# Performance work log

Hardware: AMD Instinct MI355X
Metric: run time of the kernel (lower is better)

The kernel has to match this reference:

```python
import jax, jax.numpy as jnp
from jax import lax
import numpy as np

IMG_H = 14; IMG_W = 14
L = 21   # num_labels
M = 5    # num_mixture_filters
KL = 50  # local conv kernel
PL = 25  # local conv padding
HO = IMG_H + 2 * PL - KL + 1  # 15, locally-connected output size
CH = [(64, 3), (64, 64), (128, 64), (128, 128), (256, 128), (256, 256), (256, 256),
      (512, 256), (512, 512), (512, 512), (512, 512), (512, 512), (512, 512)]
DIL = [1, 1, 1, 1, 1, 1, 1, 1, 1, 1, 2, 2, 2]


def setup_inputs() -> dict:
    keys = iter(jax.random.split(jax.random.key(0), 80))
    def rnd(shape, s=0.05):
        return jax.random.normal(next(keys), shape, dtype=jnp.float32) * s
    d = {"x": jax.random.normal(next(keys), (2, 3, IMG_H, IMG_W), dtype=jnp.float32)}
    for i, (o, c) in enumerate(CH):
        d["w%d" % (i + 1)] = rnd((o, c, 3, 3))
        d["b%d" % (i + 1)] = rnd((o,))
    d["wf1"] = rnd((4096, 512, 7, 7), s=0.01); d["bf1"] = rnd((4096,))
    d["wf2"] = rnd((4096, 4096, 1, 1), s=0.01); d["bf2"] = rnd((4096,))
    d["wf3"] = rnd((L, 4096, 1, 1), s=0.01); d["bf3"] = rnd((L,))
    d["wl"] = rnd((HO, HO, L, L, KL, KL), s=0.01)  # per-position local-conv weights
    d["bl"] = rnd((L, HO, HO))
    d["wa"] = rnd((L, L)); d["ba"] = rnd((L,))
    d["wm"] = rnd((L * M, L, 9, 9, L)); d["bm"] = rnd((L * M,))
    d["wb"] = rnd((L * M, L * M)); d["bb"] = rnd((L * M,))
    return d


def _conv2d(x, w, b, pad, dil=1):
    y = lax.conv_general_dilated(x, w, (1, 1), [(pad, pad), (pad, pad)],
                                 rhs_dilation=(dil, dil),
                                 dimension_numbers=("NCHW", "OIHW", "NCHW"))
    return y + b[None, :, None, None]


def _maxpool2(x):
    return lax.reduce_window(x, -jnp.inf, lax.max, (1, 1, 2, 2), (1, 1, 2, 2), "VALID")


def _upsample_bilinear_ac(x, H, W):
    # UpsamplingBilinear2d == bilinear with align_corners=True
    def lerp(t, n_in, n_out, axis):
        src = jnp.arange(n_out, dtype=jnp.float32) * (float(n_in - 1) / max(n_out - 1, 1))
        i0 = jnp.clip(jnp.floor(src).astype(jnp.int32), 0, max(n_in - 2, 0))
        i1 = jnp.minimum(i0 + 1, n_in - 1)
        f = src - i0.astype(jnp.float32)
        shp = [1] * t.ndim; shp[axis] = n_out
        f = f.reshape(shp).astype(t.dtype)
        return jnp.take(t, i0, axis=axis) * (1 - f) + jnp.take(t, i1, axis=axis) * f
    return lerp(lerp(x, x.shape[2], H, 2), x.shape[3], W, 3)


def reference(x, w1, b1, w2, b2, w3, b3, w4, b4, w5, b5, w6, b6, w7, b7, w8, b8,
              w9, b9, w10, b10, w11, b11, w12, b12, w13, b13,
              wf1, bf1, wf2, bf2, wf3, bf3, wl, bl, wa, ba, wm, bm, wb, bb):
    ws = [w1, w2, w3, w4, w5, w6, w7, w8, w9, w10, w11, w12, w13]
    bs = [b1, b2, b3, b4, b5, b6, b7, b8, b9, b10, b11, b12, b13]
    h = x
    for i in range(13):
        h = jax.nn.relu(_conv2d(h, ws[i], bs[i], pad=DIL[i], dil=DIL[i]))
        if i in (1, 3, 6):  # MaxPool2d after VGG blocks 1,2,3
            h = _maxpool2(h)
    h = jax.nn.relu(_conv2d(h, wf1, bf1, pad=12, dil=4))  # 7x7 dilated FC-conv
    h = jax.nn.relu(_conv2d(h, wf2, bf2, pad=0))
    h = _conv2d(h, wf3, bf3, pad=0)                       # -> [B, L, h', w']
    h = jax.nn.sigmoid(_upsample_bilinear_ac(h, IMG_H, IMG_W))
    # Conv2dLocal: locally-connected 50x50 conv, per-position weights
    xp = jnp.pad(h, ((0, 0), (0, 0), (PL, PL), (PL, PL)))
    idx = jnp.arange(HO)[:, None] + jnp.arange(KL)[None, :]  # [HO, KL]
    p = xp[:, :, idx, :][:, :, :, :, idx]  # [B, C, HO, KL, HO, KL]
    h = jnp.einsum("bcisjt,ijocst->boij", p, wl) + bl[None]  # [B, L, HO, HO]
    # Linear over the label (channel) axis
    h = jnp.einsum("bchw,oc->bohw", h, wa) + ba[None, :, None, None]
    # Conv3d mixture head: label axis unsqueezed to depth-1 last spatial dim,
    # kernel (9, 9, L) with padding (4, 4, L//2) -> depth out = 1
    y = lax.conv_general_dilated(h[..., None], wm, (1, 1, 1),
                                 [(4, 4), (4, 4), (L // 2, L // 2)],
                                 dimension_numbers=("NCDHW", "OIDHW", "NCDHW"))
    h = y[..., 0] + bm[None, :, None, None]  # [B, L*M, HO, HO]
    h = jnp.einsum("bchw,oc->bohw", h, wb) + bb[None, :, None, None]
    # BlockMinPooling(kernel=M) over last dim: split into (M, W//M), min over block axis
    B_, C_, H_, W_ = h.shape
    h = h.reshape(B_, C_, H_, M, W_ // M).min(axis=3)  # [B, L*M, HO, HO//M]
    # AvgPool2d(kernel=1, stride=1, divisor_override=1) is the identity
    return jax.nn.softmax(h, axis=1)
```

## Files before the change

kernel.cpp:

```cpp
#include <hip/hip_runtime.h>
#include <math.h>

#define HO 15
#define LBL 21
#define MIX 5
#define LM 105
#define NB 256
#define NT 512
#define GSZ (NB * NT)
#define NWV (GSZ / 64)

struct Params {
    const float* x;
    const float* w[14]; const float* b[14];
    const float *wf1, *bf1, *wf2, *bf2, *wf3, *bf3;
    const float *wl, *bl, *wa, *ba, *wm, *bm, *wb, *bb;
    float *A, *B, *v, *h1, *h3, *out;
    int* bar;
};

__device__ __forceinline__ float max4(float a, float b, float c, float d) {
    return fmaxf(fmaxf(a, b), fmaxf(c, d));
}

__device__ __forceinline__ void gbar(int* bar, int id) {
    __syncthreads();
    if (threadIdx.x == 0) {
        __threadfence();
        int* c = bar + id * 16;
        __hip_atomic_fetch_add(c, 1, __ATOMIC_RELAXED, __HIP_MEMORY_SCOPE_AGENT);
        while (__hip_atomic_load(c, __ATOMIC_RELAXED, __HIP_MEMORY_SCOPE_AGENT) < NB)
            __builtin_amdgcn_s_sleep(16);
        (void)__hip_atomic_load(c, __ATOMIC_ACQUIRE, __HIP_MEMORY_SCOPE_AGENT);
    }
    __syncthreads();
}

template <int Cin, int Cout, int Hi, int H, int POOL>
__device__ void wconv(const float* __restrict__ in, const float* __restrict__ w,
                      const float* __restrict__ bias, float* __restrict__ out,
                      int gw, int lane) {
    constexpr int CPL = Cin / 64;
    for (int idx = gw; idx < 2 * Cout * H * H; idx += NWV) {
        int x = idx % H; int t = idx / H;
        int y = t % H; t /= H;
        int o = t % Cout; int b = t / Cout;
        const float* ip = in + (size_t)b * Cin * Hi * Hi;
        float acc = 0.f;
#pragma unroll
        for (int cc = 0; cc < CPL; ++cc) {
            int c = lane + 64 * cc;
            const float* ic = ip + (size_t)c * Hi * Hi;
            const float* wc = w + ((size_t)o * Cin + c) * 9;
#pragma unroll
            for (int ky = 0; ky < 3; ++ky) {
                int yy = y + ky - 1;
                if (yy < 0 || yy >= H) continue;
#pragma unroll
                for (int kx = 0; kx < 3; ++kx) {
                    int xx = x + kx - 1;
                    if (xx < 0 || xx >= H) continue;
                    float val;
                    if (POOL == 1) {
                        val = ic[yy * Hi + xx];
                    } else {
                        const float* q = ic + (2 * yy) * Hi + 2 * xx;
                        val = max4(q[0], q[1], q[Hi], q[Hi + 1]);
                    }
                    acc += val * wc[ky * 3 + kx];
                }
            }
        }
#pragma unroll
        for (int off = 32; off; off >>= 1) acc += __shfl_xor(acc, off);
        if (lane == 0) out[idx] = fmaxf(acc + bias[o], 0.f);
    }
}

template <int Cin, int ACT, int POOLIN>
__device__ void mvtap(const float* __restrict__ in, const float* __restrict__ w,
                      const float* __restrict__ bias, float* __restrict__ out,
                      int Cout, int S, int F, float* sin, int tid, int gw, int lane) {
    if (POOLIN) {
        for (int c = tid; c < 2 * Cin; c += NT) {
            const float* q = in + (size_t)c * 9;
            sin[c] = max4(q[0], q[1], q[3], q[4]);
        }
    } else {
        for (int c = tid; c < 2 * Cin; c += NT) sin[c] = in[c];
    }
    __syncthreads();
    constexpr int K = Cin / 64;
    for (int o = gw; o < Cout; o += NWV) {
        const float* wp = w + ((size_t)o * Cin + lane) * S + F;
        float wr[K];
#pragma unroll
        for (int k = 0; k < K; ++k) wr[k] = wp[(size_t)(64 * S) * k];
        float a0 = 0.f, a1 = 0.f;
#pragma unroll
        for (int k = 0; k < K; ++k) {
            a0 += wr[k] * sin[lane + 64 * k];
            a1 += wr[k] * sin[Cin + lane + 64 * k];
        }
#pragma unroll
        for (int off = 32; off; off >>= 1) {
            a0 += __shfl_xor(a0, off);
            a1 += __shfl_xor(a1, off);
        }
        if (lane == 0) {
            float bv = bias[o];
            a0 += bv; a1 += bv;
            if (ACT == 1) { a0 = fmaxf(a0, 0.f); a1 = fmaxf(a1, 0.f); }
            if (ACT == 2) { a0 = 1.f / (1.f + expf(-a0)); a1 = 1.f / (1.f + expf(-a1)); }
            out[o] = a0;
            out[Cout + o] = a1;
        }
    }
}

template <int Cin, int ACT>
__device__ void mvrow4(const float* __restrict__ in, const float* __restrict__ w,
                       const float* __restrict__ bias, float* __restrict__ out,
                       int Cout, float* sin, int tid, int gw, int lane) {
    for (int c = tid; c < 2 * Cin; c += NT) sin[c] = in[c];
    __syncthreads();
    constexpr int K4 = Cin / 256;
    const float4* s0 = (const float4*)sin;
    const float4* s1 = (const float4*)(sin + Cin);
    for (int o = gw; o < Cout; o += NWV) {
        const float4* wp = (const float4*)(w + (size_t)o * Cin) + lane;
        float4 wr[K4];
#pragma unroll
        for (int k = 0; k < K4; ++k) wr[k] = wp[64 * k];
        float a0 = 0.f, a1 = 0.f;
#pragma unroll
        for (int k = 0; k < K4; ++k) {
            float4 xv = s0[lane + 64 * k];
            float4 yv = s1[lane + 64 * k];
            a0 += wr[k].x * xv.x + wr[k].y * xv.y + wr[k].z * xv.z + wr[k].w * xv.w;
            a1 += wr[k].x * yv.x + wr[k].y * yv.y + wr[k].z * yv.z + wr[k].w * yv.w;
        }
#pragma unroll
        for (int off = 32; off; off >>= 1) {
            a0 += __shfl_xor(a0, off);
            a1 += __shfl_xor(a1, off);
        }
        if (lane == 0) {
            float bv = bias[o];
            a0 += bv; a1 += bv;
            if (ACT == 1) { a0 = fmaxf(a0, 0.f); a1 = fmaxf(a1, 0.f); }
            if (ACT == 2) { a0 = 1.f / (1.f + expf(-a0)); a1 = 1.f / (1.f + expf(-a1)); }
            out[o] = a0;
            out[Cout + o] = a1;
        }
    }
}

__device__ void localstage(const float* __restrict__ wl, const float* __restrict__ bl,
                           const float* __restrict__ v, float* __restrict__ h1,
                           int gw, int lane) {
    int e1 = lane + 64, e2 = lane + 128, e3 = lane + 192;
    int off0 = (lane / 14) * 50 + lane % 14;
    int off1 = (e1 / 14) * 50 + e1 % 14;
    int off2 = (e2 / 14) * 50 + e2 % 14;
    int off3 = (lane < 4) ? ((e3 / 14) * 50 + e3 % 14) : off0;
    float m3 = (lane < 4) ? 1.f : 0.f;
    for (int wk = gw; wk < LBL * HO * HO; wk += NWV) {
        int j = wk % HO; int t1 = wk / HO;
        int i = t1 % HO; int o = t1 / HO;
        int s0 = 25 - i, t0 = 25 - j;
        size_t base_ij = ((size_t)(i * HO + j) * LBL + o) * LBL;
        const float* pij = wl + base_ij * 2500 + s0 * 50 + t0;
        float a0 = 0.f, a1 = 0.f;
#pragma unroll 7
        for (int c = 0; c < LBL; ++c) {
            const float* p = pij + (size_t)c * 2500;
            float part = p[off0] + p[off1] + p[off2] + m3 * p[off3];
            a0 += v[c] * part;
            a1 += v[LBL + c] * part;
        }
#pragma unroll
        for (int off = 32; off; off >>= 1) {
            a0 += __shfl_xor(a0, off);
            a1 += __shfl_xor(a1, off);
        }
        if (lane == 0) {
            float bv = bl[(o * HO + i) * HO + j];
            h1[(size_t)(0 * LBL + o) * 225 + i * HO + j] = a0 + bv;
            h1[(size_t)(1 * LBL + o) * 225 + i * HO + j] = a1 + bv;
        }
    }
}

__device__ void ninestage(const float* __restrict__ h1, const float* __restrict__ wa,
                          const float* __restrict__ ba, const float* __restrict__ wm,
                          const float* __restrict__ bm, float* __restrict__ h3,
                          float* smem, int tid) {
    int blk = blockIdx.x;
    if (blk >= 2 * LM) return;
    float* s1 = smem;
    float* s2 = smem + 4725;
    float* sw = smem + 9450;
    float* swa = smem + 11151;
    int b = blk / LM, o = blk % LM;
    for (int k = tid; k < 4725; k += NT) s1[k] = h1[(size_t)b * 4725 + k];
    for (int k = tid; k < 441; k += NT) swa[k] = wa[k];
    for (int k = tid; k < 1701; k += NT) sw[k] = wm[((size_t)o * 1701 + k) * LBL + 10];
    __syncthreads();
    for (int k = tid; k < 4725; k += NT) {
        int c = k / 225, pix = k % 225;
        float acc = ba[c];
#pragma unroll 7
        for (int c2 = 0; c2 < LBL; ++c2)
            acc += swa[c * LBL + c2] * s1[c2 * 225 + pix];
        s2[k] = acc;
    }
    __syncthreads();
    if (tid >= 225) return;
    int i = tid / HO, j = tid % HO;
    float acc = bm[o];
    for (int c = 0; c < LBL; ++c) {
        const float* wp = sw + c * 81;
        const float* hp = s2 + c * 225;
#pragma unroll
        for (int di = 0; di < 9; ++di) {
            int y = i + di - 4;
            if (y < 0 || y >= HO) continue;
#pragma unroll
            for (int dj = 0; dj < 9; ++dj) {
                int x = j + dj - 4;
                if (x < 0 || x >= HO) continue;
                acc += hp[y * HO + x] * wp[di * 9 + dj];
            }
        }
    }
    h3[((size_t)b * LM + o) * 225 + tid] = acc;
}

__device__ void finalstage(const float* __restrict__ h3, const float* __restrict__ wbw,
                           const float* __restrict__ bbv, float* __restrict__ out,
                           float* smem, int tid) {
    int blk = blockIdx.x;
    if (blk >= 2 * HO * 3) return;
    float* sv = smem;
    float* sred = smem + 112;
    int k = blk % 3; int t = blk / 3; int i = t % HO; int b = t / HO;
    int o = tid;
    if (o < LM) {
        float mn = 3.4e38f;
        for (int mm = 0; mm < MIX; ++mm) {
            int j = mm * 3 + k;
            float acc = bbv[o];
            const float* hp = h3 + (size_t)b * LM * 225 + i * HO + j;
            const float* wp = wbw + o * LM;
#pragma unroll 5
            for (int c = 0; c < LM; ++c) acc += wp[c] * hp[(size_t)c * 225];
            mn = fminf(mn, acc);
        }
        sv[o] = mn;
    }
    __syncthreads();
    if (tid < 64) {
        float m = -3.4e38f;
        for (int c = tid; c < LM; c += 64) m = fmaxf(m, sv[c]);
#pragma unroll
        for (int off = 32; off; off >>= 1) m = fmaxf(m, __shfl_xor(m, off));
        if (tid == 0) sred[0] = m;
    }
    __syncthreads();
    if (o < LM) sv[o] = expf(sv[o] - sred[0]);
    __syncthreads();
    if (tid < 64) {
        float s = 0.f;
        for (int c = tid; c < LM; c += 64) s += sv[c];
#pragma unroll
        for (int off = 32; off; off >>= 1) s += __shfl_xor(s, off);
        if (tid == 0) sred[1] = s;
    }
    __syncthreads();
    if (o < LM) out[(((size_t)b * LM + o) * HO + i) * 3 + k] = sv[o] / sred[1];
}

__global__ __launch_bounds__(NT, 1) void mega(Params p) {
    const int tid = threadIdx.x;
    const int gtid = blockIdx.x * NT + tid;
    const int gw = gtid >> 6;
    const int lane = tid & 63;
    __shared__ float smem[11592];

    for (int idx = gtid; idx < 2 * 64 * 196; idx += GSZ) {
        int x = idx % 14; int t = idx / 14;
        int y = t % 14; t /= 14;
        int o = t % 64; int b = t / 64;
        const float* ip = p.x + (size_t)b * 3 * 196;
        const float* wp = p.w[1] + (size_t)o * 27;
        float acc = p.b[1][o];
#pragma unroll
        for (int c = 0; c < 3; ++c) {
            const float* ic = ip + c * 196;
            const float* wc = wp + c * 9;
#pragma unroll
            for (int ky = 0; ky < 3; ++ky) {
                int yy = y + ky - 1;
                if (yy < 0 || yy >= 14) continue;
#pragma unroll
                for (int kx = 0; kx < 3; ++kx) {
                    int xx = x + kx - 1;
                    if (xx < 0 || xx >= 14) continue;
                    acc += ic[yy * 14 + xx] * wc[ky * 3 + kx];
                }
            }
        }
        p.A[idx] = fmaxf(acc, 0.f);
    }
    gbar(p.bar, 0);

    wconv<64,  64, 14, 14, 1>(p.A, p.w[2], p.b[2], p.B, gw, lane);  gbar(p.bar, 1);
    wconv<64, 128, 14,  7, 2>(p.B, p.w[3], p.b[3], p.A, gw, lane);  gbar(p.bar, 2);
    wconv<128,128,  7,  7, 1>(p.A, p.w[4], p.b[4], p.B, gw, lane);  gbar(p.bar, 3);
    wconv<128,256,  7,  3, 2>(p.B, p.w[5], p.b[5], p.A, gw, lane);  gbar(p.bar, 4);
    wconv<256,256,  3,  3, 1>(p.A, p.w[6], p.b[6], p.B, gw, lane);  gbar(p.bar, 5);
    wconv<256,256,  3,  3, 1>(p.B, p.w[7], p.b[7], p.A, gw, lane);  gbar(p.bar, 6);

    mvtap<256, 1, 1>(p.A, p.w[8],  p.b[8],  p.B, 512, 9, 4, smem, tid, gw, lane);   gbar(p.bar, 7);
    mvtap<512, 1, 0>(p.B, p.w[9],  p.b[9],  p.A, 512, 9, 4, smem, tid, gw, lane);   gbar(p.bar, 8);
    mvtap<512, 1, 0>(p.A, p.w[10], p.b[10], p.B, 512, 9, 4, smem, tid, gw, lane);   gbar(p.bar, 9);
    mvtap<512, 1, 0>(p.B, p.w[11], p.b[11], p.A, 512, 9, 4, smem, tid, gw, lane);   gbar(p.bar, 10);
    mvtap<512, 1, 0>(p.A, p.w[12], p.b[12], p.B, 512, 9, 4, smem, tid, gw, lane);   gbar(p.bar, 11);
    mvtap<512, 1, 0>(p.B, p.w[13], p.b[13], p.A, 512, 9, 4, smem, tid, gw, lane);   gbar(p.bar, 12);
    mvtap<512, 1, 0>(p.A, p.wf1, p.bf1, p.B, 4096, 49, 24, smem, tid, gw, lane);    gbar(p.bar, 13);
    mvrow4<4096, 1>(p.B, p.wf2, p.bf2, p.A, 4096, smem, tid, gw, lane);             gbar(p.bar, 14);
    mvrow4<4096, 2>(p.A, p.wf3, p.bf3, p.v, 21, smem, tid, gw, lane);               gbar(p.bar, 15);

    localstage(p.wl, p.bl, p.v, p.h1, gw, lane);                     gbar(p.bar, 16);
    ninestage(p.h1, p.wa, p.ba, p.wm, p.bm, p.h3, smem, tid);        gbar(p.bar, 17);
    finalstage(p.h3, p.wb, p.bb, p.out, smem, tid);
}

extern "C" void kernel_launch(void* const* d_in, const int* in_sizes, int n_in,
                              void* d_out, int out_size, void* d_ws, size_t ws_size,
                              hipStream_t stream) {
    Params p;
    p.x = (const float*)d_in[0];
    for (int i = 1; i <= 13; ++i) {
        p.w[i] = (const float*)d_in[2 * i - 1];
        p.b[i] = (const float*)d_in[2 * i];
    }
    p.wf1 = (const float*)d_in[27]; p.bf1 = (const float*)d_in[28];
    p.wf2 = (const float*)d_in[29]; p.bf2 = (const float*)d_in[30];
    p.wf3 = (const float*)d_in[31]; p.bf3 = (const float*)d_in[32];
    p.wl  = (const float*)d_in[33]; p.bl  = (const float*)d_in[34];
    p.wa  = (const float*)d_in[35]; p.ba  = (const float*)d_in[36];
    p.wm  = (const float*)d_in[37]; p.bm  = (const float*)d_in[38];
    p.wb  = (const float*)d_in[39]; p.bb  = (const float*)d_in[40];

    float* wsf = (float*)d_ws;
    p.bar = (int*)d_ws;
    p.A  = wsf + 1024;
    p.B  = wsf + 1024 + 32768;
    p.v  = wsf + 1024 + 65536;
    p.h1 = wsf + 1024 + 65600;
    p.h3 = wsf + 1024 + 75072;
    p.out = (float*)d_out;

    hipMemsetAsync(d_ws, 0, 4096, stream);
    hipLaunchKernelGGL(mega, dim3(NB), dim3(NT), 0, stream, p);
}
```

Measured before the change: 630.2 us.

## Stream whole weight rows with float4 loads instead of strided tap gathers

The 1x1-spatial conv and fc1 stages now read every weight row contiguously as float4 and keep only the centre-tap element, in place of strided scalar gathers. The locally-connected stage does the same: it streams an aligned span of each 50x50 kernel and masks to the 14x14 window. The mixture-weight load reads whole rows and keeps every 21st element. This swaps poorly coalesced sparse accesses for coalesced bulk reads, at the cost of fetching many more bytes (about 9x, 49x and 21x more for the respective weights) and more index arithmetic.

```diff
diff --git a/kernel.cpp b/kernel.cpp
--- a/kernel.cpp
+++ b/kernel.cpp
@@ -77,10 +77,10 @@
     }
 }
 
-template <int Cin, int ACT, int POOLIN>
-__device__ void mvtap(const float* __restrict__ in, const float* __restrict__ w,
-                      const float* __restrict__ bias, float* __restrict__ out,
-                      int Cout, int S, int F, float* sin, int tid, int gw, int lane) {
+template <int Cin, int S, int F, int ACT, int POOLIN>
+__device__ void mvstream(const float* __restrict__ in, const float* __restrict__ w,
+                         const float* __restrict__ bias, float* __restrict__ out,
+                         int Cout, float* sin, int tid, int gw, int lane) {
     if (POOLIN) {
         for (int c = tid; c < 2 * Cin; c += NT) {
             const float* q = in + (size_t)c * 9;
@@ -90,17 +90,22 @@
         for (int c = tid; c < 2 * Cin; c += NT) sin[c] = in[c];
     }
     __syncthreads();
-    constexpr int K = Cin / 64;
+    constexpr int N4 = Cin * S / 4;
     for (int o = gw; o < Cout; o += NWV) {
-        const float* wp = w + ((size_t)o * Cin + lane) * S + F;
-        float wr[K];
-#pragma unroll
-        for (int k = 0; k < K; ++k) wr[k] = wp[(size_t)(64 * S) * k];
+        const float4* row = (const float4*)(w + (size_t)o * Cin * S);
         float a0 = 0.f, a1 = 0.f;
-#pragma unroll
-        for (int k = 0; k < K; ++k) {
-            a0 += wr[k] * sin[lane + 64 * k];
-            a1 += wr[k] * sin[Cin + lane + 64 * k];
+#pragma unroll 4
+        for (int u = lane; u < N4; u += 64) {
+            float4 wv = row[u];
+            int b4 = 4 * u;
+            int m = F - b4 % S;
+            if (m < 0) m += S;
+            if (m < 4) {
+                int c = (b4 + m) / S;
+                float wvm = (m == 0) ? wv.x : (m == 1) ? wv.y : (m == 2) ? wv.z : wv.w;
+                a0 += wvm * sin[c];
+                a1 += wvm * sin[Cin + c];
+            }
         }
 #pragma unroll
         for (int off = 32; off; off >>= 1) {
@@ -129,16 +134,14 @@
     const float4* s1 = (const float4*)(sin + Cin);
     for (int o = gw; o < Cout; o += NWV) {
         const float4* wp = (const float4*)(w + (size_t)o * Cin) + lane;
-        float4 wr[K4];
-#pragma unroll
-        for (int k = 0; k < K4; ++k) wr[k] = wp[64 * k];
         float a0 = 0.f, a1 = 0.f;
 #pragma unroll
         for (int k = 0; k < K4; ++k) {
+            float4 wv = wp[64 * k];
             float4 xv = s0[lane + 64 * k];
             float4 yv = s1[lane + 64 * k];
-            a0 += wr[k].x * xv.x + wr[k].y * xv.y + wr[k].z * xv.z + wr[k].w * xv.w;
-            a1 += wr[k].x * yv.x + wr[k].y * yv.y + wr[k].z * yv.z + wr[k].w * yv.w;
+            a0 += wv.x * xv.x + wv.y * xv.y + wv.z * xv.z + wv.w * xv.w;
+            a1 += wv.x * yv.x + wv.y * yv.y + wv.z * yv.z + wv.w * yv.w;
         }
 #pragma unroll
         for (int off = 32; off; off >>= 1) {
@@ -159,25 +162,29 @@
 __device__ void localstage(const float* __restrict__ wl, const float* __restrict__ bl,
                            const float* __restrict__ v, float* __restrict__ h1,
                            int gw, int lane) {
-    int e1 = lane + 64, e2 = lane + 128, e3 = lane + 192;
-    int off0 = (lane / 14) * 50 + lane % 14;
-    int off1 = (e1 / 14) * 50 + e1 % 14;
-    int off2 = (e2 / 14) * 50 + e2 % 14;
-    int off3 = (lane < 4) ? ((e3 / 14) * 50 + e3 % 14) : off0;
-    float m3 = (lane < 4) ? 1.f : 0.f;
     for (int wk = gw; wk < LBL * HO * HO; wk += NWV) {
         int j = wk % HO; int t1 = wk / HO;
         int i = t1 % HO; int o = t1 / HO;
         int s0 = 25 - i, t0 = 25 - j;
+        int start = s0 * 50 + t0;
+        int af = start & ~3;
+        int n4 = (start + 664 - af + 3) >> 2;
         size_t base_ij = ((size_t)(i * HO + j) * LBL + o) * LBL;
-        const float* pij = wl + base_ij * 2500 + s0 * 50 + t0;
         float a0 = 0.f, a1 = 0.f;
-#pragma unroll 7
         for (int c = 0; c < LBL; ++c) {
-            const float* p = pij + (size_t)c * 2500;
-            float part = p[off0] + p[off1] + p[off2] + m3 * p[off3];
-            a0 += v[c] * part;
-            a1 += v[LBL + c] * part;
+            const float4* blk = (const float4*)(wl + (base_ij + c) * 2500 + af);
+            float s = 0.f;
+#pragma unroll 2
+            for (int u = lane; u < n4; u += 64) {
+                float4 wv = blk[u];
+                int p = af + 4 * u;
+                int tA = p % 50;       s += ((unsigned)(tA - t0) < 14u) ? wv.x : 0.f;
+                int tB = (p + 1) % 50; s += ((unsigned)(tB - t0) < 14u) ? wv.y : 0.f;
+                int tC = (p + 2) % 50; s += ((unsigned)(tC - t0) < 14u) ? wv.z : 0.f;
+                int tD = (p + 3) % 50; s += ((unsigned)(tD - t0) < 14u) ? wv.w : 0.f;
+            }
+            a0 += v[c] * s;
+            a1 += v[LBL + c] * s;
         }
 #pragma unroll
         for (int off = 32; off; off >>= 1) {
@@ -205,7 +212,13 @@
     int b = blk / LM, o = blk % LM;
     for (int k = tid; k < 4725; k += NT) s1[k] = h1[(size_t)b * 4725 + k];
     for (int k = tid; k < 441; k += NT) swa[k] = wa[k];
-    for (int k = tid; k < 1701; k += NT) sw[k] = wm[((size_t)o * 1701 + k) * LBL + 10];
+    {
+        const float* row = wm + (size_t)o * (1701 * 21);
+        for (int u = tid; u < 1701 * 21; u += NT) {
+            float wv = row[u];
+            if (u % 21 == 10) sw[u / 21] = wv;
+        }
+    }
     __syncthreads();
     for (int k = tid; k < 4725; k += NT) {
         int c = k / 225, pix = k % 225;
@@ -322,15 +335,15 @@
     wconv<256,256,  3,  3, 1>(p.A, p.w[6], p.b[6], p.B, gw, lane);  gbar(p.bar, 5);
     wconv<256,256,  3,  3, 1>(p.B, p.w[7], p.b[7], p.A, gw, lane);  gbar(p.bar, 6);
 
-    mvtap<256, 1, 1>(p.A, p.w[8],  p.b[8],  p.B, 512, 9, 4, smem, tid, gw, lane);   gbar(p.bar, 7);
-    mvtap<512, 1, 0>(p.B, p.w[9],  p.b[9],  p.A, 512, 9, 4, smem, tid, gw, lane);   gbar(p.bar, 8);
-    mvtap<512, 1, 0>(p.A, p.w[10], p.b[10], p.B, 512, 9, 4, smem, tid, gw, lane);   gbar(p.bar, 9);
-    mvtap<512, 1, 0>(p.B, p.w[11], p.b[11], p.A, 512, 9, 4, smem, tid, gw, lane);   gbar(p.bar, 10);
-    mvtap<512, 1, 0>(p.A, p.w[12], p.b[12], p.B, 512, 9, 4, smem, tid, gw, lane);   gbar(p.bar, 11);
-    mvtap<512, 1, 0>(p.B, p.w[13], p.b[13], p.A, 512, 9, 4, smem, tid, gw, lane);   gbar(p.bar, 12);
-    mvtap<512, 1, 0>(p.A, p.wf1, p.bf1, p.B, 4096, 49, 24, smem, tid, gw, lane);    gbar(p.bar, 13);
-    mvrow4<4096, 1>(p.B, p.wf2, p.bf2, p.A, 4096, smem, tid, gw, lane);             gbar(p.bar, 14);
-    mvrow4<4096, 2>(p.A, p.wf3, p.bf3, p.v, 21, smem, tid, gw, lane);               gbar(p.bar, 15);
+    mvstream<256, 9, 4, 1, 1>(p.A, p.w[8],  p.b[8],  p.B, 512, smem, tid, gw, lane);  gbar(p.bar, 7);
+    mvstream<512, 9, 4, 1, 0>(p.B, p.w[9],  p.b[9],  p.A, 512, smem, tid, gw, lane);  gbar(p.bar, 8);
+    mvstream<512, 9, 4, 1, 0>(p.A, p.w[10], p.b[10], p.B, 512, smem, tid, gw, lane);  gbar(p.bar, 9);
+    mvstream<512, 9, 4, 1, 0>(p.B, p.w[11], p.b[11], p.A, 512, smem, tid, gw, lane);  gbar(p.bar, 10);
+    mvstream<512, 9, 4, 1, 0>(p.A, p.w[12], p.b[12], p.B, 512, smem, tid, gw, lane);  gbar(p.bar, 11);
+    mvstream<512, 9, 4, 1, 0>(p.B, p.w[13], p.b[13], p.A, 512, smem, tid, gw, lane);  gbar(p.bar, 12);
+    mvstream<512, 49, 24, 1, 0>(p.A, p.wf1, p.bf1, p.B, 4096, smem, tid, gw, lane);   gbar(p.bar, 13);
+    mvrow4<4096, 1>(p.B, p.wf2, p.bf2, p.A, 4096, smem, tid, gw, lane);               gbar(p.bar, 14);
+    mvrow4<4096, 2>(p.A, p.wf3, p.bf3, p.v, 21, smem, tid, gw, lane);                 gbar(p.bar, 15);
 
     localstage(p.wl, p.bl, p.v, p.h1, gw, lane);                     gbar(p.bar, 16);
     ninestage(p.h1, p.wa, p.ba, p.wm, p.bm, p.h3, smem, tid);        gbar(p.bar, 17);
```

New measurement: 814.5 us. +29.2%, slower.

## Coalesce weight reads in fc1, local conv, and spread small-Cout matvecs across CUs

Applied to the files above, without the earlier changes.

Adds an mvstream path for fc1 that reads each full weight row with contiguous float4 loads and keeps only the center-tap element, replacing strided scalar gathers. The local-connected stage now has 4 lanes per kernel row, each doing one float4 load with masking, instead of scattered scalar loads. Matvecs with fewer outputs than waves spread those outputs across the grid, and mvrow4 no longer preloads all weights into registers. The fc1 change reads about 49x more bytes than it uses in exchange for coalescing, and misaligned float4 loads may be a risk in localstage.

```diff
diff --git a/kernel.cpp b/kernel.cpp
--- a/kernel.cpp
+++ b/kernel.cpp
@@ -91,7 +91,11 @@
     }
     __syncthreads();
     constexpr int K = Cin / 64;
-    for (int o = gw; o < Cout; o += NWV) {
+    int step = (Cout < NWV) ? (NWV / Cout) : 1;
+    for (int u = gw; u < Cout * step; u += NWV) {
+        if (step > 1 && (u % step) != 0) continue;
+        int o = u / step;
+        if (o >= Cout) continue;
         const float* wp = w + ((size_t)o * Cin + lane) * S + F;
         float wr[K];
 #pragma unroll
@@ -118,6 +122,44 @@
     }
 }
 
+template <int Cin, int S, int F, int ACT>
+__device__ void mvstream(const float* __restrict__ in, const float* __restrict__ w,
+                         const float* __restrict__ bias, float* __restrict__ out,
+                         int Cout, float* sin, int tid, int gw, int lane) {
+    for (int c = tid; c < 2 * Cin; c += NT) sin[c] = in[c];
+    __syncthreads();
+    constexpr int N4 = Cin * S / 4;
+    for (int o = gw; o < Cout; o += NWV) {
+        const float4* row = (const float4*)(w + (size_t)o * Cin * S);
+        float a0 = 0.f, a1 = 0.f;
+#pragma unroll 4
+        for (int u = lane; u < N4; u += 64) {
+            float4 wv = row[u];
+            int b4 = 4 * u;
+            int m = F - b4 % S;
+            if (m < 0) m += S;
+            if (m < 4) {
+                int c = (b4 + m) / S;
+                float wvm = (m == 0) ? wv.x : (m == 1) ? wv.y : (m == 2) ? wv.z : wv.w;
+                a0 += wvm * sin[c];
+                a1 += wvm * sin[Cin + c];
+            }
+        }
+#pragma unroll
+        for (int off = 32; off; off >>= 1) {
+            a0 += __shfl_xor(a0, off);
+            a1 += __shfl_xor(a1, off);
+        }
+        if (lane == 0) {
+            float bv = bias[o];
+            a0 += bv; a1 += bv;
+            if (ACT == 1) { a0 = fmaxf(a0, 0.f); a1 = fmaxf(a1, 0.f); }
+            out[o] = a0;
+            out[Cout + o] = a1;
+        }
+    }
+}
+
 template <int Cin, int ACT>
 __device__ void mvrow4(const float* __restrict__ in, const float* __restrict__ w,
                        const float* __restrict__ bias, float* __restrict__ out,
@@ -127,18 +169,20 @@
     constexpr int K4 = Cin / 256;
     const float4* s0 = (const float4*)sin;
     const float4* s1 = (const float4*)(sin + Cin);
-    for (int o = gw; o < Cout; o += NWV) {
+    int step = (Cout < NWV) ? (NWV / Cout) : 1;
+    for (int u = gw; u < Cout * step; u += NWV) {
+        if (step > 1 && (u % step) != 0) continue;
+        int o = u / step;
+        if (o >= Cout) continue;
         const float4* wp = (const float4*)(w + (size_t)o * Cin) + lane;
-        float4 wr[K4];
-#pragma unroll
-        for (int k = 0; k < K4; ++k) wr[k] = wp[64 * k];
         float a0 = 0.f, a1 = 0.f;
 #pragma unroll
         for (int k = 0; k < K4; ++k) {
+            float4 wv = wp[64 * k];
             float4 xv = s0[lane + 64 * k];
             float4 yv = s1[lane + 64 * k];
-            a0 += wr[k].x * xv.x + wr[k].y * xv.y + wr[k].z * xv.z + wr[k].w * xv.w;
-            a1 += wr[k].x * yv.x + wr[k].y * yv.y + wr[k].z * yv.z + wr[k].w * yv.w;
+            a0 += wv.x * xv.x + wv.y * xv.y + wv.z * xv.z + wv.w * xv.w;
+            a1 += wv.x * yv.x + wv.y * yv.y + wv.z * yv.z + wv.w * yv.w;
         }
 #pragma unroll
         for (int off = 32; off; off >>= 1) {
@@ -159,30 +203,40 @@
 __device__ void localstage(const float* __restrict__ wl, const float* __restrict__ bl,
                            const float* __restrict__ v, float* __restrict__ h1,
                            int gw, int lane) {
-    int e1 = lane + 64, e2 = lane + 128, e3 = lane + 192;
-    int off0 = (lane / 14) * 50 + lane % 14;
-    int off1 = (e1 / 14) * 50 + e1 % 14;
-    int off2 = (e2 / 14) * 50 + e2 % 14;
-    int off3 = (lane < 4) ? ((e3 / 14) * 50 + e3 % 14) : off0;
-    float m3 = (lane < 4) ? 1.f : 0.f;
+    int r = lane >> 2;
+    int q = lane & 3;
+    bool rv = r < 14;
+    int rc = rv ? r : 13;
     for (int wk = gw; wk < LBL * HO * HO; wk += NWV) {
         int j = wk % HO; int t1 = wk / HO;
         int i = t1 % HO; int o = t1 / HO;
         int s0 = 25 - i, t0 = 25 - j;
+        int s = s0 + rc;
+        int rowstart = s * 50 + t0;
+        int shift = rowstart & 3;
+        int off = (rowstart & ~3) + 4 * q;
+        int rel = 4 * q - shift;
+        bool tail = (q == 3) && (shift == 3) && rv;
         size_t base_ij = ((size_t)(i * HO + j) * LBL + o) * LBL;
-        const float* pij = wl + base_ij * 2500 + s0 * 50 + t0;
         float a0 = 0.f, a1 = 0.f;
 #pragma unroll 7
         for (int c = 0; c < LBL; ++c) {
-            const float* p = pij + (size_t)c * 2500;
-            float part = p[off0] + p[off1] + p[off2] + m3 * p[off3];
-            a0 += v[c] * part;
-            a1 += v[LBL + c] * part;
-        }
-#pragma unroll
-        for (int off = 32; off; off >>= 1) {
-            a0 += __shfl_xor(a0, off);
-            a1 += __shfl_xor(a1, off);
+            const float* blk = wl + (base_ij + c) * 2500;
+            float4 wv = *(const float4*)(blk + off);
+            float ssum = 0.f;
+            ssum += ((unsigned)(rel + 0) < 14u) ? wv.x : 0.f;
+            ssum += ((unsigned)(rel + 1) < 14u) ? wv.y : 0.f;
+            ssum += ((unsigned)(rel + 2) < 14u) ? wv.z : 0.f;
+            ssum += ((unsigned)(rel + 3) < 14u) ? wv.w : 0.f;
+            if (tail) ssum += blk[rowstart + 13];
+            ssum = rv ? ssum : 0.f;
+            a0 += v[c] * ssum;
+            a1 += v[LBL + c] * ssum;
+        }
+#pragma unroll
+        for (int off2 = 32; off2; off2 >>= 1) {
+            a0 += __shfl_xor(a0, off2);
+            a1 += __shfl_xor(a1, off2);
         }
         if (lane == 0) {
             float bv = bl[(o * HO + i) * HO + j];
@@ -328,7 +382,7 @@
     mvtap<512, 1, 0>(p.B, p.w[11], p.b[11], p.A, 512, 9, 4, smem, tid, gw, lane);   gbar(p.bar, 10);
     mvtap<512, 1, 0>(p.A, p.w[12], p.b[12], p.B, 512, 9, 4, smem, tid, gw, lane);   gbar(p.bar, 11);
     mvtap<512, 1, 0>(p.B, p.w[13], p.b[13], p.A, 512, 9, 4, smem, tid, gw, lane);   gbar(p.bar, 12);
-    mvtap<512, 1, 0>(p.A, p.wf1, p.bf1, p.B, 4096, 49, 24, smem, tid, gw, lane);    gbar(p.bar, 13);
+    mvstream<512, 49, 24, 1>(p.A, p.wf1, p.bf1, p.B, 4096, smem, tid, gw, lane);    gbar(p.bar, 13);
     mvrow4<4096, 1>(p.B, p.wf2, p.bf2, p.A, 4096, smem, tid, gw, lane);             gbar(p.bar, 14);
     mvrow4<4096, 2>(p.A, p.wf3, p.bf3, p.v, 21, smem, tid, gw, lane);               gbar(p.bar, 15);
 
```

Measured after the change: 727.4 us. 1.15x slower.
